# Performance work log

Hardware: AMD Instinct MI355X
Metric: run time of the kernel (lower is better)

## Reference

```python
import jax, jax.numpy as jnp
import numpy as np

B, T, C, H = 8, 1024, 768, 12
HD = C // H  # head_dim = 64


def setup_inputs() -> dict:
    key = jax.random.key(0)
    ks = jax.random.split(key, 5)
    x = jax.random.normal(ks[0], (B, T, C), dtype=jnp.float32)
    mask = jnp.tril(jnp.ones((T, T), dtype=bool))[None, None, :, :]  # causal [1,1,T,T]
    # Dense params (flax Dense: y = x @ kernel + bias)
    W_qkv = jax.random.normal(ks[1], (C, 3 * C), dtype=jnp.float32) * (1.0 / np.sqrt(C))
    b_qkv = jnp.zeros((3 * C,), dtype=jnp.float32)
    W_proj = jax.random.normal(ks[2], (C, C), dtype=jnp.float32) * (1.0 / np.sqrt(C))
    b_proj = jnp.zeros((C,), dtype=jnp.float32)
    return {"x": x, "mask": mask, "W_qkv": W_qkv, "b_qkv": b_qkv,
            "W_proj": W_proj, "b_proj": b_proj}


def reference(x, mask, W_qkv, b_qkv, W_proj, b_proj):
    Bx, Tx, Cx = x.shape
    qkv = x @ W_qkv + b_qkv                      # [B, T, 3C]
    qkv = qkv.reshape(Bx, Tx, 3 * H, HD)
    q, k, v = jnp.array_split(qkv, 3, axis=2)    # each [B, T, H, HD]
    scale = 1.0 / jnp.sqrt(jnp.float32(HD))
    attn = jnp.einsum('bqhd,bkhd->bhqk', q, k) * scale  # [B, H, T, T]
    attn = jnp.where(mask, attn, jnp.finfo(jnp.float32).min)
    attn = jax.nn.softmax(attn, axis=-1)
    out = jnp.einsum('bhqk,bkhd->bqhd', attn, v).reshape(Bx, Tx, Cx)
    return out @ W_proj + b_proj
```

## Files before the change

### kernel.cpp

```cpp
#include <hip/hip_runtime.h>


typedef unsigned short u16;
typedef unsigned int u32;
typedef __bf16 bf16x8 __attribute__((ext_vector_type(8)));
typedef float  f32x4  __attribute__((ext_vector_type(4)));
typedef float  f32x16 __attribute__((ext_vector_type(16)));
typedef unsigned short u16x4 __attribute__((ext_vector_type(4)));
typedef unsigned short u16x8 __attribute__((ext_vector_type(8)));
typedef unsigned int u32x4 __attribute__((ext_vector_type(4)));

#define DEV static __device__ __forceinline__

constexpr int B_ = 8, T_ = 1024, C_ = 768, H_ = 12, HD_ = 64;
constexpr int M1 = B_ * T_;
constexpr int N1 = 3 * C_;
constexpr int KD = C_;

DEV u16 f2bf(float f) {
    union { float f; unsigned u; } v; v.f = f;
    unsigned r = v.u + 0x7fffu + ((v.u >> 16) & 1u);
    return (u16)(r >> 16);
}

DEV u16 bfbits(float f) {
    __bf16 h = (__bf16)f;
    union { __bf16 h; u16 u; } v; v.h = h;
    return v.u;
}

DEV u32 cvtpk(float lo, float hi) {
    u32 r;
    asm("v_cvt_pk_bf16_f32 %0, %1, %2" : "=v"(r) : "v"(lo), "v"(hi));
    return r;
}

DEV void gload16(const void* g, void* l) {
    __builtin_amdgcn_global_load_lds(
        (const __attribute__((address_space(1))) unsigned*)g,
        (__attribute__((address_space(3))) unsigned*)l, 16, 0, 0);
}

DEV float redmax16(f32x16 v) {
    float a0 = fmaxf(v[0], v[1]), a1 = fmaxf(v[2], v[3]);
    float a2 = fmaxf(v[4], v[5]), a3 = fmaxf(v[6], v[7]);
    float a4 = fmaxf(v[8], v[9]), a5 = fmaxf(v[10], v[11]);
    float a6 = fmaxf(v[12], v[13]), a7 = fmaxf(v[14], v[15]);
    float b0 = fmaxf(a0, a1), b1 = fmaxf(a2, a3);
    float b2 = fmaxf(a4, a5), b3 = fmaxf(a6, a7);
    return fmaxf(fmaxf(b0, b1), fmaxf(b2, b3));
}
DEV float redsum16(f32x16 v) {
    float a0 = v[0] + v[1], a1 = v[2] + v[3], a2 = v[4] + v[5], a3 = v[6] + v[7];
    float a4 = v[8] + v[9], a5 = v[10] + v[11], a6 = v[12] + v[13], a7 = v[14] + v[15];
    float b0 = a0 + a1, b1 = a2 + a3, b2 = a4 + a5, b3 = a6 + a7;
    return (b0 + b1) + (b2 + b3);
}


__global__ __launch_bounds__(256) void cvt_x_kern(const float* __restrict__ x,
                                                  u16* __restrict__ xb, int n8) {
    int i = blockIdx.x * 256 + threadIdx.x;
    if (i >= n8) return;
    const float4* xf = (const float4*)x;
    float4 a = xf[i * 2], b = xf[i * 2 + 1];
    u16x8 o;
    o[0] = f2bf(a.x); o[1] = f2bf(a.y); o[2] = f2bf(a.z); o[3] = f2bf(a.w);
    o[4] = f2bf(b.x); o[5] = f2bf(b.y); o[6] = f2bf(b.z); o[7] = f2bf(b.w);
    *(u16x8*)(xb + (size_t)i * 8) = o;
}

__global__ __launch_bounds__(256) void cvt_w_kern(const float* __restrict__ Wq,
                                                  const float* __restrict__ Wp,
                                                  u16* __restrict__ WqT,
                                                  u16* __restrict__ WpT) {
    __shared__ float tile[32][33];
    int bx = blockIdx.x;
    const float* W; u16* Wt; int N;
    if (bx < N1 / 32) { W = Wq; Wt = WqT; N = N1; }
    else { bx -= N1 / 32; W = Wp; Wt = WpT; N = C_; }
    int n0 = bx * 32, k0 = blockIdx.y * 32;
    int tx = threadIdx.x & 31, ty = threadIdx.x >> 5;
#pragma unroll
    for (int i = 0; i < 4; i++) {
        int k = ty * 4 + i;
        tile[k][tx] = W[(size_t)(k0 + k) * N + n0 + tx];
    }
    __syncthreads();
#pragma unroll
    for (int i = 0; i < 4; i++) {
        int n = ty * 4 + i;
        Wt[(size_t)(n0 + n) * KD + k0 + tx] = f2bf(tile[tx][n]);
    }
}


template <int MODE>
__global__ __launch_bounds__(256, 2) void gemm_bt_kern(
    const u16* __restrict__ A, const u16* __restrict__ Bt,
    const float* __restrict__ bias, int nBN,
    u16* __restrict__ qw, u16* __restrict__ kw, u16* __restrict__ vw,
    float* __restrict__ out) {
    __shared__ u16 lds[16384];
    char* LA = (char*)lds;
    char* LB = (char*)lds + 16384;
    const int cpx = gridDim.x >> 3;
    const int bid = (blockIdx.x & 7) * cpx + (blockIdx.x >> 3);
    const int bm = bid / nBN, bn = bid % nBN;
    const int m0 = bm * 128, n0 = bn * 128;
    const int t = threadIdx.x;
    const int lane = t & 63, w = t >> 6;
    const int wr = w >> 1, wc = w & 1;
    const int l15 = lane & 15, lhi = lane >> 4;
    const int srow = t >> 3;
    const int scb = ((t & 7) << 4) ^ ((srow & 7) << 4);
    const char* Ab = (const char*)(A + (size_t)(m0 + srow) * KD) + scb;
    const char* Bb = (const char*)(Bt + (size_t)(n0 + srow) * KD) + scb;

    f32x4 acc[4][4] = {};

    for (int k0 = 0; k0 < KD; k0 += 64) {
#pragma unroll
        for (int s = 0; s < 4; s++) {
            gload16(Ab + (size_t)k0 * 2 + (size_t)s * 32 * KD * 2, LA + w * 1024 + s * 4096);
            gload16(Bb + (size_t)k0 * 2 + (size_t)s * 32 * KD * 2, LB + w * 1024 + s * 4096);
        }
        __syncthreads();
#pragma unroll
        for (int kk = 0; kk < 2; kk++) {
            bf16x8 af[4], bfr[4];
#pragma unroll
            for (int i = 0; i < 4; i++) {
                int rowA = wr * 64 + i * 16 + l15;
                af[i] = *(const bf16x8*)(LA + rowA * 128 +
                                         ((kk * 64 + lhi * 16) ^ ((rowA & 7) << 4)));
                int rowB = wc * 64 + i * 16 + l15;
                bfr[i] = *(const bf16x8*)(LB + rowB * 128 +
                                          ((kk * 64 + lhi * 16) ^ ((rowB & 7) << 4)));
            }
#pragma unroll
            for (int fm = 0; fm < 4; fm++)
#pragma unroll
                for (int fn = 0; fn < 4; fn++)
                    acc[fm][fn] = __builtin_amdgcn_mfma_f32_16x16x32_bf16(
                        af[fm], bfr[fn], acc[fm][fn], 0, 0, 0);
        }
        __syncthreads();
    }

    if constexpr (MODE == 1) {
#pragma unroll
        for (int fm = 0; fm < 4; fm++) {
            const int mb = m0 + wr * 64 + fm * 16 + lhi * 4;
#pragma unroll
            for (int fn = 0; fn < 4; fn++) {
                const int n = n0 + wc * 64 + fn * 16 + l15;
                const float bv = bias[n];
#pragma unroll
                for (int r = 0; r < 4; r++)
                    out[(size_t)(mb + r) * C_ + n] = acc[fm][fn][r] + bv;
            }
        }
    } else {
        char* TT = (char*)lds;
        const int typ = bn / 6;
        const int h0 = (bn % 6) * 2;
        if (typ < 2) {
            const float sc = (typ == 0) ? 0.125f * 1.44269504f : 1.0f;
#pragma unroll
            for (int fn = 0; fn < 4; fn++) {
                const int col = wc * 64 + fn * 16 + l15;
                const float bv = bias[n0 + col];
#pragma unroll
                for (int fm = 0; fm < 4; fm++) {
                    const int row0 = wr * 64 + fm * 16 + lhi * 4;
#pragma unroll
                    for (int r = 0; r < 4; r++) {
                        const int row = row0 + r;
                        *(u16*)(TT + row * 256 + ((col * 2) ^ ((row & 7) << 5))) =
                            bfbits((acc[fm][fn][r] + bv) * sc);
                    }
                }
            }
            __syncthreads();
            u16* dst = (typ == 0) ? qw : kw;
#pragma unroll
            for (int i = 0; i < 8; i++) {
                const int wk = t + 256 * i;
                const int m = wk >> 4, c = wk & 15;
                u16x8 v8 = *(u16x8*)(TT + m * 256 + ((c * 16) ^ ((m & 7) << 5)));
                const int mb = m0 + m, b = mb >> 10, tq = mb & 1023;
                const int h = h0 + (c >> 3), d0 = (c & 7) * 8;
                *(u16x8*)(dst + (((size_t)(b * H_ + h) * T_ + tq) << 6) + d0) = v8;
            }
        } else {
#pragma unroll
            for (int fn = 0; fn < 4; fn++) {
                const int col = wc * 64 + fn * 16 + l15;
                const float bv = bias[n0 + col];
                const int cx = (col & 7) << 4;
#pragma unroll
                for (int fm = 0; fm < 4; fm++) {
                    const int row0 = wr * 64 + fm * 16 + lhi * 4;
                    u16x4 pk;
#pragma unroll
                    for (int r = 0; r < 4; r++) pk[r] = bfbits(acc[fm][fn][r] + bv);
                    *(u16x4*)(TT + col * 256 + ((row0 * 2) ^ cx)) = pk;
                }
            }
            __syncthreads();
#pragma unroll
            for (int i = 0; i < 8; i++) {
                const int wk = t + 256 * i;
                const int col = wk >> 4, ch = wk & 15;
                u16x8 v8 = *(u16x8*)(TT + col * 256 + ((ch * 16) ^ ((col & 7) << 4)));
                const int b = m0 >> 10, tq0 = (m0 & 1023) + ch * 8;
                const int h = h0 + (col >> 6), d = col & 63;
                *(u16x8*)(vw + (((size_t)(b * H_ + h) * HD_ + d) << 10) + tq0) = v8;
            }
        }
    }
}


__global__ __launch_bounds__(256, 4) void attn_fwd_kern(
    const u16* __restrict__ qg, const u16* __restrict__ kg,
    const u16* __restrict__ vg, u16* __restrict__ ao) {
    __shared__ u16 kld[2][64 * 64];
    __shared__ u16 vld[2][64 * 64];
    const int n = blockIdx.x;
    const int bh = (n & 7) + 8 * ((n >> 3) % 12);
    const int qt = 7 - n / 96;
    const int t = threadIdx.x, lane = t & 63, w = t >> 6;
    const int q5 = lane & 31, h2 = lane >> 5;
    const int srow = t >> 3;
    const int scb = ((t & 7) << 4) ^ ((srow & 7) << 4);
    const char* kb = (const char*)(kg + (size_t)bh * T_ * HD_);
    const char* vb = (const char*)(vg + (size_t)bh * HD_ * T_);

    const int qrow_g = qt * 128 + w * 32 + q5;
    const u16* qrow = qg + (size_t)bh * T_ * HD_ + (size_t)qrow_g * HD_ + h2 * 8;
    bf16x8 qf[4];
#pragma unroll
    for (int kc = 0; kc < 4; kc++)
        qf[kc] = *(const bf16x8*)(qrow + kc * 16);

#pragma unroll
    for (int s = 0; s < 2; s++) {
        gload16(kb + (size_t)(srow + s * 32) * 128 + scb,
                (char*)kld[0] + w * 1024 + s * 4096);
        gload16(vb + (size_t)(srow + s * 32) * 2048 + scb,
                (char*)vld[0] + w * 1024 + s * 4096);
    }
    __syncthreads();

    f32x16 acc[2] = {};
    float mst = -1e30f, lst = 0.f;
    const int qmax = qt * 128 + w * 32 + 31;

    const int ntiles = 2 * qt + 2;
    for (int kvt = 0; kvt < ntiles; kvt++) {
        const int cur = kvt & 1;
        if (kvt + 1 < ntiles) {
#pragma unroll
            for (int s = 0; s < 2; s++) {
                gload16(kb + (size_t)((kvt + 1) * 64 + srow + s * 32) * 128 + scb,
                        (char*)kld[cur ^ 1] + w * 1024 + s * 4096);
                gload16(vb + (size_t)(srow + s * 32) * 2048 + (kvt + 1) * 128 + scb,
                        (char*)vld[cur ^ 1] + w * 1024 + s * 4096);
            }
        }
        if (kvt * 64 <= qmax) {
            const char* kbase = (const char*)kld[cur];
            const char* vbase = (const char*)vld[cur];
            f32x16 s0 = {}, s1 = {};
            __builtin_amdgcn_s_setprio(1);
#pragma unroll
            for (int kc = 0; kc < 4; kc++) {
                const int r0 = q5, r1 = 32 + q5;
                bf16x8 kf0 = *(const bf16x8*)(kbase + r0 * 128 +
                                              ((kc * 32 + h2 * 16) ^ ((r0 & 7) << 4)));
                bf16x8 kf1 = *(const bf16x8*)(kbase + r1 * 128 +
                                              ((kc * 32 + h2 * 16) ^ ((r1 & 7) << 4)));
                s0 = __builtin_amdgcn_mfma_f32_32x32x16_bf16(kf0, qf[kc], s0, 0, 0, 0);
                s1 = __builtin_amdgcn_mfma_f32_32x32x16_bf16(kf1, qf[kc], s1, 0, 0, 0);
            }
            __builtin_amdgcn_s_setprio(0);
            if (kvt * 64 + 63 > qt * 128 + w * 32) {
                const int qg_ = qrow_g, kvb0 = kvt * 64 + 4 * h2;
#pragma unroll
                for (int r = 0; r < 16; r++) {
                    const int kvo = (r & 3) + 8 * (r >> 2);
                    if (kvb0 + kvo > qg_) s0[r] = -1e30f;
                    if (kvb0 + 32 + kvo > qg_) s1[r] = -1e30f;
                }
            }
            float pmax = fmaxf(redmax16(s0), redmax16(s1));
            pmax = fmaxf(pmax, __shfl_xor(pmax, 32));
            if (!__all(pmax <= mst)) {
                const float mn = fmaxf(mst, pmax);
                const float corr = exp2f(mst - mn);
                mst = mn;
#pragma unroll
                for (int r = 0; r < 16; r++) { acc[0][r] *= corr; acc[1][r] *= corr; }
                lst *= corr;
            }
#pragma unroll
            for (int r = 0; r < 16; r++) {
                s0[r] = exp2f(s0[r] - mst);
                s1[r] = exp2f(s1[r] - mst);
            }
            float rs = redsum16(s0) + redsum16(s1);
            rs += __shfl_xor(rs, 32);
            lst += rs;
            u32 pw0[8], pw1[8];
#pragma unroll
            for (int i = 0; i < 4; i++) {
                pw0[i]     = cvtpk(s0[4 * i + 0], s0[4 * i + 1]);
                pw1[i]     = cvtpk(s0[4 * i + 2], s0[4 * i + 3]);
                pw0[i + 4] = cvtpk(s1[4 * i + 0], s1[4 * i + 1]);
                pw1[i + 4] = cvtpk(s1[4 * i + 2], s1[4 * i + 3]);
            }
            bf16x8 pf[4];
#pragma unroll
            for (int m = 0; m < 4; m++) {
                u32 a0 = pw0[2 * m], b0 = pw0[2 * m + 1];
                asm("v_permlane32_swap_b32 %0, %1" : "+v"(a0), "+v"(b0));
                u32 a1 = pw1[2 * m], b1 = pw1[2 * m + 1];
                asm("v_permlane32_swap_b32 %0, %1" : "+v"(a1), "+v"(b1));
                u32x4 wv; wv[0] = a0; wv[1] = a1; wv[2] = b0; wv[3] = b1;
                pf[m] = __builtin_bit_cast(bf16x8, wv);
            }
            __builtin_amdgcn_s_setprio(1);
#pragma unroll
            for (int m = 0; m < 4; m++) {
#pragma unroll
                for (int db = 0; db < 2; db++) {
                    const int rd = db * 32 + q5;
                    bf16x8 vf = *(const bf16x8*)(vbase + rd * 128 +
                                                 ((m * 32 + h2 * 16) ^ ((rd & 7) << 4)));
                    acc[db] = __builtin_amdgcn_mfma_f32_32x32x16_bf16(vf, pf[m], acc[db], 0, 0, 0);
                }
            }
            __builtin_amdgcn_s_setprio(0);
        }
        __syncthreads();
    }

    const int b = bh / H_, h = bh % H_;
    const float inv = 1.0f / lst;
    u16* orow = ao + (size_t)(b * T_ + qrow_g) * C_ + h * 64 + 4 * h2;
#pragma unroll
    for (int db = 0; db < 2; db++)
#pragma unroll
        for (int q2 = 0; q2 < 4; q2++) {
            u16x4 pk;
#pragma unroll
            for (int e = 0; e < 4; e++) pk[e] = bfbits(acc[db][q2 * 4 + e] * inv);
            *(u16x4*)(orow + db * 32 + q2 * 8) = pk;
        }
}


extern "C" void kernel_launch(void* const* d_in, const int* in_sizes, int n_in,
                              void* d_out, int out_size, void* d_ws, size_t ws_size,
                              hipStream_t stream) {
    const float* x     = (const float*)d_in[0];
    const float* Wqkv  = (const float*)d_in[2];
    const float* bqkv  = (const float*)d_in[3];
    const float* Wproj = (const float*)d_in[4];
    const float* bproj = (const float*)d_in[5];
    float* out = (float*)d_out;

    char* ws = (char*)d_ws;
    u16* xb     = (u16*)(ws);
    u16* wqkvT  = (u16*)(ws + 12582912);
    u16* wprojT = (u16*)(ws + 16121856);
    u16* qw     = (u16*)(ws + 17301504);
    u16* kw     = (u16*)(ws + 29884416);
    u16* vw     = (u16*)(ws + 42467328);
    u16* ao     = (u16*)(ws + 55050240);

    cvt_x_kern<<<(M1 * C_ / 8 + 255) / 256, 256, 0, stream>>>(x, xb, M1 * C_ / 8);
    cvt_w_kern<<<dim3(N1 / 32 + C_ / 32, KD / 32), 256, 0, stream>>>(
        Wqkv, Wproj, wqkvT, wprojT);

    gemm_bt_kern<0><<<(M1 / 128) * (N1 / 128), 256, 0, stream>>>(
        xb, wqkvT, bqkv, N1 / 128, qw, kw, vw, nullptr);

    attn_fwd_kern<<<B_ * H_ * (T_ / 128), 256, 0, stream>>>(qw, kw, vw, ao);

    gemm_bt_kern<1><<<(M1 / 128) * (C_ / 128), 256, 0, stream>>>(
        ao, wprojT, bproj, C_ / 128, nullptr, nullptr, nullptr, out);
}
```

Baseline: 105.0 us.

## Double-buffer GEMM LDS staging with a 32-wide K step

Restructures the GEMM main loop so LDS holds two 16 KB buffers, each carrying a 128x32 tile of A and of B. The loads for the next K step are issued before the MFMAs on the current buffer, so global-to-LDS transfer can overlap compute. The loop keeps one barrier per step, but the step count doubles because each step covers half as much K. The swizzle changes to fit the 64-byte rows. The gain depends on how well the async loads hide latency against the extra barriers.

```diff
diff --git a/kernel.cpp b/kernel.cpp
--- a/kernel.cpp
+++ b/kernel.cpp
@@ -102,8 +102,6 @@
     u16* __restrict__ qw, u16* __restrict__ kw, u16* __restrict__ vw,
     float* __restrict__ out) {
     __shared__ u16 lds[16384];
-    char* LA = (char*)lds;
-    char* LB = (char*)lds + 16384;
     const int cpx = gridDim.x >> 3;
     const int bid = (blockIdx.x & 7) * cpx + (blockIdx.x >> 3);
     const int bm = bid / nBN, bn = bid % nBN;
@@ -112,39 +110,47 @@
     const int lane = t & 63, w = t >> 6;
     const int wr = w >> 1, wc = w & 1;
     const int l15 = lane & 15, lhi = lane >> 4;
-    const int srow = t >> 3;
-    const int scb = ((t & 7) << 4) ^ ((srow & 7) << 4);
-    const char* Ab = (const char*)(A + (size_t)(m0 + srow) * KD) + scb;
-    const char* Bb = (const char*)(Bt + (size_t)(n0 + srow) * KD) + scb;
+    const int r0 = t >> 2;
+    const int gsl = ((t & 3) ^ (r0 & 3)) << 4;
+    const char* Ab = (const char*)A + (size_t)(m0 + r0) * KD * 2 + gsl;
+    const char* Bb = (const char*)Bt + (size_t)(n0 + r0) * KD * 2 + gsl;
+
+    auto stage = [&](int buf, int k0) {
+        char* dst = (char*)lds + buf * 16384 + w * 1024;
+        const size_t ko = (size_t)k0 * 2;
+#pragma unroll
+        for (int s = 0; s < 2; s++) {
+            gload16(Ab + ko + (size_t)s * 64 * KD * 2, dst + s * 4096);
+            gload16(Bb + ko + (size_t)s * 64 * KD * 2, dst + 8192 + s * 4096);
+        }
+    };
+
+    stage(0, 0);
+    __syncthreads();
 
     f32x4 acc[4][4] = {};
-
-    for (int k0 = 0; k0 < KD; k0 += 64) {
-#pragma unroll
-        for (int s = 0; s < 4; s++) {
-            gload16(Ab + (size_t)k0 * 2 + (size_t)s * 32 * KD * 2, LA + w * 1024 + s * 4096);
-            gload16(Bb + (size_t)k0 * 2 + (size_t)s * 32 * KD * 2, LB + w * 1024 + s * 4096);
-        }
-        __syncthreads();
-#pragma unroll
-        for (int kk = 0; kk < 2; kk++) {
-            bf16x8 af[4], bfr[4];
-#pragma unroll
-            for (int i = 0; i < 4; i++) {
-                int rowA = wr * 64 + i * 16 + l15;
-                af[i] = *(const bf16x8*)(LA + rowA * 128 +
-                                         ((kk * 64 + lhi * 16) ^ ((rowA & 7) << 4)));
-                int rowB = wc * 64 + i * 16 + l15;
-                bfr[i] = *(const bf16x8*)(LB + rowB * 128 +
-                                          ((kk * 64 + lhi * 16) ^ ((rowB & 7) << 4)));
-            }
-#pragma unroll
-            for (int fm = 0; fm < 4; fm++)
-#pragma unroll
-                for (int fn = 0; fn < 4; fn++)
-                    acc[fm][fn] = __builtin_amdgcn_mfma_f32_16x16x32_bf16(
-                        af[fm], bfr[fn], acc[fm][fn], 0, 0, 0);
-        }
+    constexpr int NSTEP = KD / 32;
+    for (int st = 0; st < NSTEP; ++st) {
+        const int cur = st & 1;
+        if (st + 1 < NSTEP) stage(cur ^ 1, (st + 1) * 32);
+        const char* baseA = (const char*)lds + cur * 16384;
+        const char* baseB = baseA + 8192;
+        bf16x8 af[4], bfr[4];
+#pragma unroll
+        for (int i = 0; i < 4; i++) {
+            const int rowA = wr * 64 + i * 16 + l15;
+            af[i] = *(const bf16x8*)(baseA + rowA * 64 +
+                                     ((lhi * 16) ^ ((rowA & 3) << 4)));
+            const int rowB = wc * 64 + i * 16 + l15;
+            bfr[i] = *(const bf16x8*)(baseB + rowB * 64 +
+                                      ((lhi * 16) ^ ((rowB & 3) << 4)));
+        }
+#pragma unroll
+        for (int fm = 0; fm < 4; fm++)
+#pragma unroll
+            for (int fn = 0; fn < 4; fn++)
+                acc[fm][fn] = __builtin_amdgcn_mfma_f32_16x16x32_bf16(
+                    af[fm], bfr[fn], acc[fm][fn], 0, 0, 0);
         __syncthreads();
     }
 
```

After: 107.7 us. +2.5%, slower.

## Split attention into single-wave blocks reading K/V directly from global memory

Applied to the files above, without the earlier changes.

The attention kernel now launches one 64-thread wave per 32-query slice instead of four waves sharing a 128-query block. It drops the double-buffered LDS staging of K and V tiles and the per-tile block barriers, loading MFMA operands straight from global memory (relying on caches). Each wave also loops only over the KV tiles its own causal range needs. This removes sync and LDS overhead and balances causal work more finely, but gives up K/V reuse across waves through LDS, so global and cache traffic per FLOP rises and the loads are no longer prefetched ahead of use.

```diff
diff --git a/kernel.cpp b/kernel.cpp
--- a/kernel.cpp
+++ b/kernel.cpp
@@ -223,18 +223,16 @@
 }
 
 
-__global__ __launch_bounds__(256, 4) void attn_fwd_kern(
+__global__ __launch_bounds__(64, 4) void attn_fwd_kern(
     const u16* __restrict__ qg, const u16* __restrict__ kg,
     const u16* __restrict__ vg, u16* __restrict__ ao) {
-    __shared__ u16 kld[2][64 * 64];
-    __shared__ u16 vld[2][64 * 64];
     const int n = blockIdx.x;
     const int bh = (n & 7) + 8 * ((n >> 3) % 12);
-    const int qt = 7 - n / 96;
-    const int t = threadIdx.x, lane = t & 63, w = t >> 6;
+    const int r = n / 96;
+    const int qt = 7 - (r >> 2);
+    const int w = r & 3;
+    const int lane = threadIdx.x & 63;
     const int q5 = lane & 31, h2 = lane >> 5;
-    const int srow = t >> 3;
-    const int scb = ((t & 7) << 4) ^ ((srow & 7) << 4);
     const char* kb = (const char*)(kg + (size_t)bh * T_ * HD_);
     const char* vb = (const char*)(vg + (size_t)bh * HD_ * T_);
 
@@ -245,106 +243,79 @@
     for (int kc = 0; kc < 4; kc++)
         qf[kc] = *(const bf16x8*)(qrow + kc * 16);
 
-#pragma unroll
-    for (int s = 0; s < 2; s++) {
-        gload16(kb + (size_t)(srow + s * 32) * 128 + scb,
-                (char*)kld[0] + w * 1024 + s * 4096);
-        gload16(vb + (size_t)(srow + s * 32) * 2048 + scb,
-                (char*)vld[0] + w * 1024 + s * 4096);
-    }
-    __syncthreads();
-
     f32x16 acc[2] = {};
     float mst = -1e30f, lst = 0.f;
-    const int qmax = qt * 128 + w * 32 + 31;
-
-    const int ntiles = 2 * qt + 2;
-    for (int kvt = 0; kvt < ntiles; kvt++) {
-        const int cur = kvt & 1;
-        if (kvt + 1 < ntiles) {
-#pragma unroll
-            for (int s = 0; s < 2; s++) {
-                gload16(kb + (size_t)((kvt + 1) * 64 + srow + s * 32) * 128 + scb,
-                        (char*)kld[cur ^ 1] + w * 1024 + s * 4096);
-                gload16(vb + (size_t)(srow + s * 32) * 2048 + (kvt + 1) * 128 + scb,
-                        (char*)vld[cur ^ 1] + w * 1024 + s * 4096);
-            }
-        }
-        if (kvt * 64 <= qmax) {
-            const char* kbase = (const char*)kld[cur];
-            const char* vbase = (const char*)vld[cur];
-            f32x16 s0 = {}, s1 = {};
-            __builtin_amdgcn_s_setprio(1);
-#pragma unroll
-            for (int kc = 0; kc < 4; kc++) {
-                const int r0 = q5, r1 = 32 + q5;
-                bf16x8 kf0 = *(const bf16x8*)(kbase + r0 * 128 +
-                                              ((kc * 32 + h2 * 16) ^ ((r0 & 7) << 4)));
-                bf16x8 kf1 = *(const bf16x8*)(kbase + r1 * 128 +
-                                              ((kc * 32 + h2 * 16) ^ ((r1 & 7) << 4)));
-                s0 = __builtin_amdgcn_mfma_f32_32x32x16_bf16(kf0, qf[kc], s0, 0, 0, 0);
-                s1 = __builtin_amdgcn_mfma_f32_32x32x16_bf16(kf1, qf[kc], s1, 0, 0, 0);
-            }
-            __builtin_amdgcn_s_setprio(0);
-            if (kvt * 64 + 63 > qt * 128 + w * 32) {
-                const int qg_ = qrow_g, kvb0 = kvt * 64 + 4 * h2;
-#pragma unroll
-                for (int r = 0; r < 16; r++) {
-                    const int kvo = (r & 3) + 8 * (r >> 2);
-                    if (kvb0 + kvo > qg_) s0[r] = -1e30f;
-                    if (kvb0 + 32 + kvo > qg_) s1[r] = -1e30f;
-                }
-            }
-            float pmax = fmaxf(redmax16(s0), redmax16(s1));
-            pmax = fmaxf(pmax, __shfl_xor(pmax, 32));
-            if (!__all(pmax <= mst)) {
-                const float mn = fmaxf(mst, pmax);
-                const float corr = exp2f(mst - mn);
-                mst = mn;
-#pragma unroll
-                for (int r = 0; r < 16; r++) { acc[0][r] *= corr; acc[1][r] *= corr; }
-                lst *= corr;
-            }
-#pragma unroll
-            for (int r = 0; r < 16; r++) {
-                s0[r] = exp2f(s0[r] - mst);
-                s1[r] = exp2f(s1[r] - mst);
-            }
-            float rs = redsum16(s0) + redsum16(s1);
-            rs += __shfl_xor(rs, 32);
-            lst += rs;
-            u32 pw0[8], pw1[8];
-#pragma unroll
-            for (int i = 0; i < 4; i++) {
-                pw0[i]     = cvtpk(s0[4 * i + 0], s0[4 * i + 1]);
-                pw1[i]     = cvtpk(s0[4 * i + 2], s0[4 * i + 3]);
-                pw0[i + 4] = cvtpk(s1[4 * i + 0], s1[4 * i + 1]);
-                pw1[i + 4] = cvtpk(s1[4 * i + 2], s1[4 * i + 3]);
-            }
-            bf16x8 pf[4];
-#pragma unroll
-            for (int m = 0; m < 4; m++) {
-                u32 a0 = pw0[2 * m], b0 = pw0[2 * m + 1];
-                asm("v_permlane32_swap_b32 %0, %1" : "+v"(a0), "+v"(b0));
-                u32 a1 = pw1[2 * m], b1 = pw1[2 * m + 1];
-                asm("v_permlane32_swap_b32 %0, %1" : "+v"(a1), "+v"(b1));
-                u32x4 wv; wv[0] = a0; wv[1] = a1; wv[2] = b0; wv[3] = b1;
-                pf[m] = __builtin_bit_cast(bf16x8, wv);
-            }
-            __builtin_amdgcn_s_setprio(1);
-#pragma unroll
-            for (int m = 0; m < 4; m++) {
-#pragma unroll
-                for (int db = 0; db < 2; db++) {
-                    const int rd = db * 32 + q5;
-                    bf16x8 vf = *(const bf16x8*)(vbase + rd * 128 +
-                                                 ((m * 32 + h2 * 16) ^ ((rd & 7) << 4)));
-                    acc[db] = __builtin_amdgcn_mfma_f32_32x32x16_bf16(vf, pf[m], acc[db], 0, 0, 0);
-                }
-            }
-            __builtin_amdgcn_s_setprio(0);
-        }
-        __syncthreads();
+    const int nt = ((qt * 128 + w * 32 + 31) >> 6) + 1;
+
+    for (int kvt = 0; kvt < nt; kvt++) {
+        const char* kt = kb + (size_t)kvt * 64 * 128;
+        const char* vt = vb + (size_t)kvt * 128;
+        f32x16 s0 = {}, s1 = {};
+        __builtin_amdgcn_s_setprio(1);
+#pragma unroll
+        for (int kc = 0; kc < 4; kc++) {
+            bf16x8 kf0 = *(const bf16x8*)(kt + q5 * 128 + kc * 32 + h2 * 16);
+            bf16x8 kf1 = *(const bf16x8*)(kt + (32 + q5) * 128 + kc * 32 + h2 * 16);
+            s0 = __builtin_amdgcn_mfma_f32_32x32x16_bf16(kf0, qf[kc], s0, 0, 0, 0);
+            s1 = __builtin_amdgcn_mfma_f32_32x32x16_bf16(kf1, qf[kc], s1, 0, 0, 0);
+        }
+        __builtin_amdgcn_s_setprio(0);
+        if (kvt * 64 + 63 > qt * 128 + w * 32) {
+            const int kvb0 = kvt * 64 + 4 * h2;
+#pragma unroll
+            for (int rr = 0; rr < 16; rr++) {
+                const int kvo = (rr & 3) + 8 * (rr >> 2);
+                if (kvb0 + kvo > qrow_g) s0[rr] = -1e30f;
+                if (kvb0 + 32 + kvo > qrow_g) s1[rr] = -1e30f;
+            }
+        }
+        float pmax = fmaxf(redmax16(s0), redmax16(s1));
+        pmax = fmaxf(pmax, __shfl_xor(pmax, 32));
+        if (!__all(pmax <= mst)) {
+            const float mn = fmaxf(mst, pmax);
+            const float corr = exp2f(mst - mn);
+            mst = mn;
+#pragma unroll
+            for (int rr = 0; rr < 16; rr++) { acc[0][rr] *= corr; acc[1][rr] *= corr; }
+            lst *= corr;
+        }
+#pragma unroll
+        for (int rr = 0; rr < 16; rr++) {
+            s0[rr] = exp2f(s0[rr] - mst);
+            s1[rr] = exp2f(s1[rr] - mst);
+        }
+        float rs = redsum16(s0) + redsum16(s1);
+        rs += __shfl_xor(rs, 32);
+        lst += rs;
+        u32 pw0[8], pw1[8];
+#pragma unroll
+        for (int i = 0; i < 4; i++) {
+            pw0[i]     = cvtpk(s0[4 * i + 0], s0[4 * i + 1]);
+            pw1[i]     = cvtpk(s0[4 * i + 2], s0[4 * i + 3]);
+            pw0[i + 4] = cvtpk(s1[4 * i + 0], s1[4 * i + 1]);
+            pw1[i + 4] = cvtpk(s1[4 * i + 2], s1[4 * i + 3]);
+        }
+        bf16x8 pf[4];
+#pragma unroll
+        for (int m = 0; m < 4; m++) {
+            u32 a0 = pw0[2 * m], b0 = pw0[2 * m + 1];
+            asm("v_permlane32_swap_b32 %0, %1" : "+v"(a0), "+v"(b0));
+            u32 a1 = pw1[2 * m], b1 = pw1[2 * m + 1];
+            asm("v_permlane32_swap_b32 %0, %1" : "+v"(a1), "+v"(b1));
+            u32x4 wv; wv[0] = a0; wv[1] = a1; wv[2] = b0; wv[3] = b1;
+            pf[m] = __builtin_bit_cast(bf16x8, wv);
+        }
+        __builtin_amdgcn_s_setprio(1);
+#pragma unroll
+        for (int m = 0; m < 4; m++) {
+#pragma unroll
+            for (int db = 0; db < 2; db++) {
+                bf16x8 vf = *(const bf16x8*)(vt + (size_t)(db * 32 + q5) * 2048 +
+                                             m * 32 + h2 * 16);
+                acc[db] = __builtin_amdgcn_mfma_f32_32x32x16_bf16(vf, pf[m], acc[db], 0, 0, 0);
+            }
+        }
+        __builtin_amdgcn_s_setprio(0);
     }
 
     const int b = bh / H_, h = bh % H_;
@@ -388,7 +359,7 @@
     gemm_bt_kern<0><<<(M1 / 128) * (N1 / 128), 256, 0, stream>>>(
         xb, wqkvT, bqkv, N1 / 128, qw, kw, vw, nullptr);
 
-    attn_fwd_kern<<<B_ * H_ * (T_ / 128), 256, 0, stream>>>(qw, kw, vw, ao);
+    attn_fwd_kern<<<B_ * H_ * (T_ / 128) * 4, 64, 0, stream>>>(qw, kw, vw, ao);
 
     gemm_bt_kern<1><<<(M1 / 128) * (C_ / 128), 256, 0, stream>>>(
         ao, wprojT, bproj, C_ / 128, nullptr, nullptr, nullptr, out);
```

After: 131.9 us. 25.6% more time.
